# Kernel optimization log

Hardware: AMD Instinct MI355X
Metric: run time of the kernel (lower is better)

The kernel has to match this reference:

```python
import jax, jax.numpy as jnp
import numpy as np

IN_FEATURES = 4096
OUT_FEATURES = 1024
BATCH = 16384
WERR = 1.0
BERR = 1.0


def setup_inputs() -> dict:
    key = jax.random.key(0)
    kx, kw = jax.random.split(key)
    X = jax.random.normal(kx, (BATCH, IN_FEATURES), dtype=jnp.float32)
    # glorot_uniform init for W, zeros for bias (as in Keras layer)
    limit = np.sqrt(6.0 / (IN_FEATURES + OUT_FEATURES)).astype(np.float32)
    W = jax.random.uniform(kw, (IN_FEATURES, OUT_FEATURES), dtype=jnp.float32,
                           minval=-limit, maxval=limit)
    bias = jnp.zeros((1, OUT_FEATURES), dtype=jnp.float32)
    return {"X": X, "W": W, "bias": bias}


def reference(X, W, bias):
    # Binarize weights/bias with sign(), scaled by Werr/Berr, then dense matmul.
    Wb = jnp.sign(W) * WERR          # [in, out], values in {-1, 0, +1}
    bb = jnp.sign(bias) * BERR       # [1, out]
    Z = jnp.matmul(X, Wb) + bb       # [batch, out]
    return Z
```

## Files before the change

kernel.cpp:

```cpp
#include <hip/hip_runtime.h>

#define M_DIM 16384
#define N_DIM 1024
#define K_DIM 4096

#define BM 256
#define BN 256
#define BK 64
#define NT (K_DIM / BK)

typedef __attribute__((ext_vector_type(4))) float f32x4;
typedef __attribute__((ext_vector_type(8))) short bf16x8;
typedef __attribute__((ext_vector_type(8))) unsigned short u16x8;

static __device__ __forceinline__ short f2bf(float f) {
  union { __bf16 h; short s; } u;
  u.h = (__bf16)f;
  return u.s;
}

static __device__ __forceinline__ void load_lds16(const void* g, void* l) {
  __builtin_amdgcn_global_load_lds(
      (const __attribute__((address_space(1))) void*)g,
      (__attribute__((address_space(3))) void*)l, 16, 0, 0);
}

__global__ __launch_bounds__(256) void wsign_transpose(
    const float* __restrict__ W, unsigned short* __restrict__ WbT) {
  __shared__ unsigned short tile[64][72];
  const int t  = (int)threadIdx.x;
  const int k0 = (int)(blockIdx.x >> 4) * 64;
  const int n0 = (int)(blockIdx.x & 15) * 64;
#pragma unroll
  for (int p = 0; p < 4; ++p) {
    const int r = p * 16 + (t >> 4);
    const int c = (t & 15) * 4;
    const float* src = W + (size_t)(k0 + r) * N_DIM + n0 + c;
#pragma unroll
    for (int j = 0; j < 4; ++j) {
      const float w = src[j];
      tile[r][c + j] = (w > 0.f) ? (unsigned short)0x3F80u
                                 : ((w < 0.f) ? (unsigned short)0xBF80u
                                              : (unsigned short)0u);
    }
  }
  __syncthreads();
  const int n  = t >> 2;
  const int kg = (t & 3) * 16;
  u16x8 o0, o1;
#pragma unroll
  for (int j = 0; j < 8; ++j) o0[j] = tile[kg + j][n];
#pragma unroll
  for (int j = 0; j < 8; ++j) o1[j] = tile[kg + 8 + j][n];
  unsigned short* dst = WbT + (size_t)(n0 + n) * K_DIM + k0 + kg;
  *(u16x8*)dst       = o0;
  *(u16x8*)(dst + 8) = o1;
}

__global__ __launch_bounds__(512, 2) void gemm_8ph(
    const float* __restrict__ X, const unsigned short* __restrict__ WbT,
    const float* __restrict__ bias, float* __restrict__ Z) {
  __shared__ __align__(16) unsigned short As[2][BM * BK];
  __shared__ __align__(16) unsigned short Bs[2][BN * BK];

  const int t   = (int)threadIdx.x;
  const int l   = t & 63;
  const int wid = t >> 6;
  const int wm  = wid >> 2;
  const int wn  = wid & 3;

  const int bid = (int)blockIdx.x;
  const int swz = (bid & 7) * 32 + (bid >> 3);
  const int m0  = (swz >> 2) * BM;
  const int n0  = (swz & 3) * BN;

  const int abase = (wm * 128 + (l & 15)) * BK;
  const int bbase = (wn * 64 + (l & 15)) * BK;
  const int axk0  = (((l >> 4) + 0) ^ (l & 7)) << 3;
  const int axk1  = (((l >> 4) + 4) ^ (l & 7)) << 3;

  const float* sA[4];
#pragma unroll
  for (int i = 0; i < 4; ++i)
    sA[i] = X + (size_t)(m0 + i * 64 + (t >> 3)) * K_DIM + (t & 7) * 8;
  const int adst = (t >> 3) * BK + (((t & 7) ^ ((t >> 3) & 7)) << 3);

  const unsigned short* b_src[4];
  int b_dst[4];
#pragma unroll
  for (int i = 0; i < 4; ++i) {
    const int c = i * 512 + t;
    const int n = c >> 3, gp = c & 7;
    b_src[i] = WbT + (size_t)(n0 + n) * K_DIM + (gp ^ (n & 7)) * 8;
    b_dst[i] = c * 8;
  }

  f32x4 acc[8][4] = {};
  f32x4 ar[2][2];
  bf16x8 aF[2][4];
  bf16x8 bF0[2][2], bF1[2][2];

#define SB0 __builtin_amdgcn_sched_barrier(0)
#define BAR do { SB0; __builtin_amdgcn_s_barrier(); SB0; } while (0)
#define WVM(N) do { asm volatile("s_waitcnt vmcnt(" #N ")" ::: "memory"); SB0; } while (0)
#define WLG0 do { asm volatile("s_waitcnt lgkmcnt(0)" ::: "memory"); SB0; } while (0)

#define LD_AH(H, KT)                                                       \
  do { SB0;                                                                \
    ar[0][0] = *(const f32x4*)(sA[2 * (H)] + (KT));                        \
    ar[0][1] = *(const f32x4*)(sA[2 * (H)] + (KT) + 4);                    \
    ar[1][0] = *(const f32x4*)(sA[2 * (H) + 1] + (KT));                    \
    ar[1][1] = *(const f32x4*)(sA[2 * (H) + 1] + (KT) + 4); SB0;           \
  } while (0)
#define WR_AH(H, BUF)                                                      \
  do {                                                                     \
    _Pragma("unroll") for (int j = 0; j < 2; ++j) {                        \
      u16x8 v;                                                             \
      _Pragma("unroll") for (int q = 0; q < 4; ++q) {                      \
        v[q]     = (unsigned short)f2bf(ar[j][0][q]);                      \
        v[4 + q] = (unsigned short)f2bf(ar[j][1][q]);                      \
      }                                                                    \
      *(u16x8*)(&As[BUF][adst + (2 * (H) + j) * 4096]) = v;                \
    }                                                                      \
  } while (0)
#define DMA_B2(KT, BUF, I0)                                                \
  do { SB0;                                                                \
    _Pragma("unroll") for (int i = (I0); i < (I0) + 2; ++i)                \
      load_lds16(b_src[i] + (KT), &Bs[BUF][b_dst[i]]);                     \
    SB0;                                                                   \
  } while (0)
#define RD_A(MH, AB)                                                       \
  do { SB0;                                                                \
    _Pragma("unroll") for (int mi = 0; mi < 4; ++mi) {                     \
      aF[0][mi] = *(const bf16x8*)((AB) + abase + ((MH)*4 + mi) * 1024 + axk0); \
      aF[1][mi] = *(const bf16x8*)((AB) + abase + ((MH)*4 + mi) * 1024 + axk1); \
    } SB0;                                                                 \
  } while (0)
#define RD_B(DST, NH, BB)                                                  \
  do { SB0;                                                                \
    _Pragma("unroll") for (int nj = 0; nj < 2; ++nj) {                     \
      DST[0][nj] = *(const bf16x8*)((BB) + bbase + ((NH)*2 + nj) * 1024 + axk0); \
      DST[1][nj] = *(const bf16x8*)((BB) + bbase + ((NH)*2 + nj) * 1024 + axk1); \
    } SB0;                                                                 \
  } while (0)
#define Q(MH, NH, BF)                                                      \
  do { __builtin_amdgcn_s_setprio(1);                                      \
    _Pragma("unroll") for (int kk = 0; kk < 2; ++kk)                       \
      _Pragma("unroll") for (int mi = 0; mi < 4; ++mi)                     \
        _Pragma("unroll") for (int nj = 0; nj < 2; ++nj)                   \
          acc[(MH)*4 + mi][(NH)*2 + nj] =                                  \
              __builtin_amdgcn_mfma_f32_16x16x32_bf16(                     \
                  aF[kk][mi], BF[kk][nj], acc[(MH)*4 + mi][(NH)*2 + nj],   \
                  0, 0, 0);                                                \
    __builtin_amdgcn_s_setprio(0);                                         \
  } while (0)

  LD_AH(0, 0); WVM(0); WR_AH(0, 0);
  LD_AH(1, 0); WVM(0); WR_AH(1, 0);
  DMA_B2(0, 0, 0); DMA_B2(0, 0, 2);
  WVM(0); WLG0;
  BAR;

  for (int tt = 0; tt < NT - 1; ++tt) {
    const int cur = tt & 1, nxt = cur ^ 1;
    const unsigned short* Ab = As[cur];
    const unsigned short* Bb = Bs[cur];
    const int ktn = (tt + 1) * BK;
    RD_A(0, Ab);
    RD_B(bF0, 0, Bb);
    LD_AH(0, ktn);
    BAR; WLG0;
    Q(0, 0, bF0);
    BAR;
    RD_B(bF1, 1, Bb);
    DMA_B2(ktn, nxt, 0);
    WVM(2);
    WR_AH(0, nxt);
    BAR; WLG0;
    Q(0, 1, bF1);
    BAR;
    RD_A(1, Ab);
    LD_AH(1, ktn);
    DMA_B2(ktn, nxt, 2);
    BAR; WLG0;
    Q(1, 1, bF1);
    BAR;
    WVM(0);
    WR_AH(1, nxt);
    Q(1, 0, bF0);
    WLG0;
    BAR;
  }

  {
    const unsigned short* Ab = As[(NT - 1) & 1];
    const unsigned short* Bb = Bs[(NT - 1) & 1];
    RD_A(0, Ab);
    RD_B(bF0, 0, Bb);
    WLG0;
    Q(0, 0, bF0);
    RD_B(bF1, 1, Bb);
    WLG0;
    Q(0, 1, bF1);
    RD_A(1, Ab);
    WLG0;
    Q(1, 1, bF1);
    Q(1, 0, bF0);
  }

#pragma unroll
  for (int ni = 0; ni < 4; ++ni) {
    const int col = n0 + wn * 64 + ni * 16 + (l & 15);
    const float b  = bias[col];
    const float bs = (b > 0.f) ? 1.f : ((b < 0.f) ? -1.f : 0.f);
#pragma unroll
    for (int mi = 0; mi < 8; ++mi) {
      const int row = m0 + wm * 128 + mi * 16 + ((l >> 4) << 2);
#pragma unroll
      for (int j = 0; j < 4; ++j)
        Z[(size_t)(row + j) * N_DIM + col] = acc[mi][ni][j] + bs;
    }
  }
#undef SB0
#undef BAR
#undef WVM
#undef WLG0
#undef LD_AH
#undef WR_AH
#undef DMA_B2
#undef RD_A
#undef RD_B
#undef Q
}

__global__ __launch_bounds__(256) void naive_fb(
    const float* __restrict__ X, const float* __restrict__ W,
    const float* __restrict__ bias, float* __restrict__ Z) {
  const size_t id = (size_t)blockIdx.x * 256 + threadIdx.x;
  const int m = (int)(id >> 10), n = (int)(id & 1023);
  float acc = 0.f;
  for (int k = 0; k < K_DIM; ++k) {
    const float w = W[(size_t)k * N_DIM + n];
    const float s = (w > 0.f) ? 1.f : ((w < 0.f) ? -1.f : 0.f);
    acc += X[(size_t)m * K_DIM + k] * s;
  }
  const float b = bias[n];
  Z[id] = acc + ((b > 0.f) ? 1.f : ((b < 0.f) ? -1.f : 0.f));
}

extern "C" void kernel_launch(void* const* d_in, const int* in_sizes, int n_in,
                              void* d_out, int out_size, void* d_ws, size_t ws_size,
                              hipStream_t stream) {
  const float* X    = (const float*)d_in[0];
  const float* W    = (const float*)d_in[1];
  const float* bias = (const float*)d_in[2];
  float* Z = (float*)d_out;

  const size_t needW = (size_t)N_DIM * K_DIM * sizeof(unsigned short);
  if (ws_size >= needW) {
    unsigned short* WbT = (unsigned short*)d_ws;
    wsign_transpose<<<dim3((K_DIM / 64) * (N_DIM / 64)), dim3(256), 0, stream>>>(W, WbT);
    gemm_8ph<<<dim3((M_DIM / BM) * (N_DIM / BN)), dim3(512), 0, stream>>>(X, WbT, bias, Z);
  } else {
    naive_fb<<<dim3((size_t)M_DIM * N_DIM / 256), dim3(256), 0, stream>>>(X, W, bias, Z);
  }
}
```

Before: 202.5 us.

## Prefetch fp32 A tile two K-steps ahead with split register buffers

The A-tile global loads now run two K-iterations ahead instead of one. Two separate register buffers (ar1, ar2) hold the halves of the fp32 A tile, and the loop is restructured with a peeled penultimate iteration and adjusted vmcnt waits. This hides more of the global-load latency of the fp32 X stream behind MFMA work. In exchange it uses more VGPRs, which could cause spills under the 512x2 launch bounds.

Measured after the change: 187.1 us. 7.6% less time.

```diff
diff --git a/kernel.cpp b/kernel.cpp
--- a/kernel.cpp
+++ b/kernel.cpp
@@ -57,7 +57,7 @@
   *(u16x8*)(dst + 8) = o1;
 }
 
-__global__ __launch_bounds__(512, 2) void gemm_8ph(
+__global__ __launch_bounds__(512, 2) void gemm_p4(
     const float* __restrict__ X, const unsigned short* __restrict__ WbT,
     const float* __restrict__ bias, float* __restrict__ Z) {
   __shared__ __align__(16) unsigned short As[2][BM * BK];
@@ -79,10 +79,10 @@
   const int axk0  = (((l >> 4) + 0) ^ (l & 7)) << 3;
   const int axk1  = (((l >> 4) + 4) ^ (l & 7)) << 3;
 
-  const float* sA[4];
-#pragma unroll
-  for (int i = 0; i < 4; ++i)
-    sA[i] = X + (size_t)(m0 + i * 64 + (t >> 3)) * K_DIM + (t & 7) * 8;
+  const float* sA0 = X + (size_t)(m0 +   0 + (t >> 3)) * K_DIM + (t & 7) * 8;
+  const float* sA1 = X + (size_t)(m0 +  64 + (t >> 3)) * K_DIM + (t & 7) * 8;
+  const float* sA2 = X + (size_t)(m0 + 128 + (t >> 3)) * K_DIM + (t & 7) * 8;
+  const float* sA3 = X + (size_t)(m0 + 192 + (t >> 3)) * K_DIM + (t & 7) * 8;
   const int adst = (t >> 3) * BK + (((t & 7) ^ ((t >> 3) & 7)) << 3);
 
   const unsigned short* b_src[4];
@@ -96,7 +96,7 @@
   }
 
   f32x4 acc[8][4] = {};
-  f32x4 ar[2][2];
+  f32x4 ar1[2][2], ar2[2][2];
   bf16x8 aF[2][4];
   bf16x8 bF0[2][2], bF1[2][2];
 
@@ -105,22 +105,29 @@
 #define WVM(N) do { asm volatile("s_waitcnt vmcnt(" #N ")" ::: "memory"); SB0; } while (0)
 #define WLG0 do { asm volatile("s_waitcnt lgkmcnt(0)" ::: "memory"); SB0; } while (0)
 
-#define LD_AH(H, KT)                                                       \
-  do { SB0;                                                                \
-    ar[0][0] = *(const f32x4*)(sA[2 * (H)] + (KT));                        \
-    ar[0][1] = *(const f32x4*)(sA[2 * (H)] + (KT) + 4);                    \
-    ar[1][0] = *(const f32x4*)(sA[2 * (H) + 1] + (KT));                    \
-    ar[1][1] = *(const f32x4*)(sA[2 * (H) + 1] + (KT) + 4); SB0;           \
-  } while (0)
-#define WR_AH(H, BUF)                                                      \
+#define LD_A1(KT)                                                          \
+  do { SB0;                                                                \
+    ar1[0][0] = *(const f32x4*)(sA0 + (KT));                               \
+    ar1[0][1] = *(const f32x4*)(sA0 + (KT) + 4);                           \
+    ar1[1][0] = *(const f32x4*)(sA1 + (KT));                               \
+    ar1[1][1] = *(const f32x4*)(sA1 + (KT) + 4); SB0;                      \
+  } while (0)
+#define LD_A2(KT)                                                          \
+  do { SB0;                                                                \
+    ar2[0][0] = *(const f32x4*)(sA2 + (KT));                               \
+    ar2[0][1] = *(const f32x4*)(sA2 + (KT) + 4);                           \
+    ar2[1][0] = *(const f32x4*)(sA3 + (KT));                               \
+    ar2[1][1] = *(const f32x4*)(sA3 + (KT) + 4); SB0;                      \
+  } while (0)
+#define WR_A(AR, BUF, OFS)                                                 \
   do {                                                                     \
     _Pragma("unroll") for (int j = 0; j < 2; ++j) {                        \
       u16x8 v;                                                             \
       _Pragma("unroll") for (int q = 0; q < 4; ++q) {                      \
-        v[q]     = (unsigned short)f2bf(ar[j][0][q]);                      \
-        v[4 + q] = (unsigned short)f2bf(ar[j][1][q]);                      \
+        v[q]     = (unsigned short)f2bf(AR[j][0][q]);                      \
+        v[4 + q] = (unsigned short)f2bf(AR[j][1][q]);                      \
       }                                                                    \
-      *(u16x8*)(&As[BUF][adst + (2 * (H) + j) * 4096]) = v;                \
+      *(u16x8*)(&As[BUF][adst + (OFS) + j * 4096]) = v;                    \
     }                                                                      \
   } while (0)
 #define DMA_B2(KT, BUF, I0)                                                \
@@ -155,46 +162,77 @@
     __builtin_amdgcn_s_setprio(0);                                         \
   } while (0)
 
-  LD_AH(0, 0); WVM(0); WR_AH(0, 0);
-  LD_AH(1, 0); WVM(0); WR_AH(1, 0);
+  LD_A1(0); LD_A2(0);
+  WVM(4); WR_A(ar1, 0, 0);
+  WVM(0); WR_A(ar2, 0, 8192);
   DMA_B2(0, 0, 0); DMA_B2(0, 0, 2);
-  WVM(0); WLG0;
+  LD_A1(BK); LD_A2(BK);
+  WLG0;
   BAR;
 
-  for (int tt = 0; tt < NT - 1; ++tt) {
+  for (int tt = 0; tt < NT - 2; ++tt) {
     const int cur = tt & 1, nxt = cur ^ 1;
     const unsigned short* Ab = As[cur];
     const unsigned short* Bb = Bs[cur];
-    const int ktn = (tt + 1) * BK;
+    const int kt1 = (tt + 1) * BK, kt2 = (tt + 2) * BK;
+    WVM(8);
     RD_A(0, Ab);
     RD_B(bF0, 0, Bb);
-    LD_AH(0, ktn);
     BAR; WLG0;
     Q(0, 0, bF0);
     BAR;
+    WVM(4);
+    WR_A(ar1, nxt, 0);
     RD_B(bF1, 1, Bb);
-    DMA_B2(ktn, nxt, 0);
+    DMA_B2(kt1, nxt, 0);
+    BAR; WLG0;
+    Q(0, 1, bF1);
+    BAR;
     WVM(2);
-    WR_AH(0, nxt);
+    WR_A(ar2, nxt, 8192);
+    RD_A(1, Ab);
+    DMA_B2(kt1, nxt, 2);
+    LD_A1(kt2);
+    BAR; WLG0;
+    Q(1, 1, bF1);
+    BAR;
+    LD_A2(kt2);
+    Q(1, 0, bF0);
+    BAR;
+  }
+
+  {
+    const int cur = (NT - 2) & 1, nxt = cur ^ 1;
+    const unsigned short* Ab = As[cur];
+    const unsigned short* Bb = Bs[cur];
+    const int kt1 = (NT - 1) * BK;
+    WVM(8);
+    RD_A(0, Ab);
+    RD_B(bF0, 0, Bb);
+    BAR; WLG0;
+    Q(0, 0, bF0);
+    BAR;
+    WVM(4);
+    WR_A(ar1, nxt, 0);
+    RD_B(bF1, 1, Bb);
+    DMA_B2(kt1, nxt, 0);
     BAR; WLG0;
     Q(0, 1, bF1);
     BAR;
+    WVM(2);
+    WR_A(ar2, nxt, 8192);
     RD_A(1, Ab);
-    LD_AH(1, ktn);
-    DMA_B2(ktn, nxt, 2);
+    DMA_B2(kt1, nxt, 2);
     BAR; WLG0;
     Q(1, 1, bF1);
     BAR;
-    WVM(0);
-    WR_AH(1, nxt);
     Q(1, 0, bF0);
-    WLG0;
-    BAR;
-  }
-
+    BAR;
+  }
   {
     const unsigned short* Ab = As[(NT - 1) & 1];
     const unsigned short* Bb = Bs[(NT - 1) & 1];
+    WVM(0);
     RD_A(0, Ab);
     RD_B(bF0, 0, Bb);
     WLG0;
@@ -225,8 +263,9 @@
 #undef BAR
 #undef WVM
 #undef WLG0
-#undef LD_AH
-#undef WR_AH
+#undef LD_A1
+#undef LD_A2
+#undef WR_A
 #undef DMA_B2
 #undef RD_A
 #undef RD_B
@@ -260,7 +299,7 @@
   if (ws_size >= needW) {
     unsigned short* WbT = (unsigned short*)d_ws;
     wsign_transpose<<<dim3((K_DIM / 64) * (N_DIM / 64)), dim3(256), 0, stream>>>(W, WbT);
-    gemm_8ph<<<dim3((M_DIM / BM) * (N_DIM / BN)), dim3(512), 0, stream>>>(X, WbT, bias, Z);
+    gemm_p4<<<dim3((M_DIM / BM) * (N_DIM / BN)), dim3(512), 0, stream>>>(X, WbT, bias, Z);
   } else {
     naive_fb<<<dim3((size_t)M_DIM * N_DIM / 256), dim3(256), 0, stream>>>(X, W, bias, Z);
   }
```
